# Optimization experiments

Measured on AMD Instinct MI355X. Metric: run time of the kernel, lower is better.

Reference implementation:

```python
import jax, jax.numpy as jnp
import numpy as np


def setup_inputs() -> dict:
    key = jax.random.key(0)
    ks = jax.random.split(key, 5)
    B, S, H = 64, 1024, 1024
    scale = 1.0 / np.sqrt(H)
    return {
        "decoder_hidden": jax.random.normal(ks[0], (B, H), jnp.float32),
        "encoder_outputs": jax.random.normal(ks[1], (B, S, H), jnp.float32),
        "W1": jax.random.normal(ks[2], (H, H), jnp.float32) * scale,
        "W2": jax.random.normal(ks[3], (H, H), jnp.float32) * scale,
        "v": jax.random.normal(ks[4], (H,), jnp.float32) * scale,
    }


def reference(decoder_hidden, encoder_outputs, W1, W2, v):
    # W1 @ decoder_hidden: [B, H] computed once, broadcast over src_len
    dh_proj = jnp.einsum("bh,oh->bo", decoder_hidden, W1)          # [B, H]
    enc_proj = jnp.einsum("bsh,oh->bso", encoder_outputs, W2)      # [B, S, H]
    energy = jnp.tanh(dh_proj[:, None, :] + enc_proj)              # [B, S, H]
    scores = jnp.einsum("bsh,h->bs", energy, v)                    # [B, S]
    attention_weights = jax.nn.softmax(scores, axis=-1)            # [B, S]
    context = jnp.einsum("bs,bsh->bh", attention_weights, encoder_outputs)
    return (context, attention_weights)
```

## Files before the change

### kernel.cpp

```cpp
#include <hip/hip_runtime.h>
#include <hip/hip_bf16.h>
#include <cmath>

#define Hdim 1024
#define Bdim 64
#define Sdim 1024

typedef __attribute__((ext_vector_type(4))) float f32x4;
typedef __attribute__((ext_vector_type(8))) short s16x8;
typedef __attribute__((ext_vector_type(4))) unsigned int u32x4;

static __device__ __forceinline__ unsigned short f2bf(float f) {
  unsigned int u = __builtin_bit_cast(unsigned int, f);
  unsigned int r = (u + 0x7fffu + ((u >> 16) & 1u)) >> 16;
  return (unsigned short)r;
}

static __device__ __forceinline__ float bf2f(unsigned short u) {
  return __builtin_bit_cast(float, (unsigned int)u << 16);
}

#define TANH_C 2.885390081777927f


static __device__ __forceinline__ void stage_rows64(const float* __restrict__ src,
                                                    unsigned short* As, int tid) {
  #pragma unroll 4
  for (int i = 0; i < 32; ++i) {
    int c = tid + i * 256;
    int row = c >> 7;
    int k8 = (c & 127) << 3;
    const float4* p = reinterpret_cast<const float4*>(src + row * Hdim + k8);
    float4 a = p[0];
    float4 b = p[1];
    union { unsigned short us[8]; u32x4 v; } pk;
    pk.us[0] = f2bf(a.x); pk.us[1] = f2bf(a.y); pk.us[2] = f2bf(a.z); pk.us[3] = f2bf(a.w);
    pk.us[4] = f2bf(b.x); pk.us[5] = f2bf(b.y); pk.us[6] = f2bf(b.z); pk.us[7] = f2bf(b.w);
    int idx = row * Hdim + (k8 ^ ((row & 7) << 3));
    *reinterpret_cast<u32x4*>(&As[idx]) = pk.v;
  }
}

static __device__ __forceinline__ s16x8 lda_full(const unsigned short* As, int row, int k) {
  int idx = row * Hdim + (k ^ ((row & 7) << 3));
  return *reinterpret_cast<const s16x8*>(&As[idx]);
}

static __device__ __forceinline__ s16x8 ldb_g(const unsigned short* __restrict__ Wb,
                                              const float* __restrict__ Wf,
                                              int use_bf, int o, int k) {
  if (use_bf) {
    return *reinterpret_cast<const s16x8*>(&Wb[o * Hdim + k]);
  } else {
    const float4* p = reinterpret_cast<const float4*>(Wf + o * Hdim + k);
    float4 a = p[0];
    float4 b = p[1];
    union { unsigned short us[8]; s16x8 v; } pk;
    pk.us[0] = f2bf(a.x); pk.us[1] = f2bf(a.y); pk.us[2] = f2bf(a.z); pk.us[3] = f2bf(a.w);
    pk.us[4] = f2bf(b.x); pk.us[5] = f2bf(b.y); pk.us[6] = f2bf(b.z); pk.us[7] = f2bf(b.w);
    return pk.v;
  }
}

__global__ void cast_bf16_kernel(const float* __restrict__ src,
                                 unsigned short* __restrict__ dst) {
  int i = blockIdx.x * 256 + threadIdx.x;
  const float4* p = reinterpret_cast<const float4*>(src) + i * 2;
  float4 a = p[0];
  float4 b = p[1];
  union { unsigned short us[8]; u32x4 v; } pk;
  pk.us[0] = f2bf(a.x); pk.us[1] = f2bf(a.y); pk.us[2] = f2bf(a.z); pk.us[3] = f2bf(a.w);
  pk.us[4] = f2bf(b.x); pk.us[5] = f2bf(b.y); pk.us[6] = f2bf(b.z); pk.us[7] = f2bf(b.w);
  *reinterpret_cast<u32x4*>(dst + i * 8) = pk.v;
}

__global__ __launch_bounds__(256, 1) void proj_kernel(
    const float* __restrict__ dh, const float* __restrict__ W1f,
    const unsigned short* __restrict__ W1b, float* __restrict__ out, int use_bf) {
  __shared__ unsigned short As[64 * Hdim];
  int tid = threadIdx.x;
  stage_rows64(dh, As, tid);
  __syncthreads();
  int w = tid >> 6, lane = tid & 63;
  int lo = lane & 15, hi = lane >> 4;
  int o = blockIdx.x * 16 + lo;
  f32x4 acc = {0.f, 0.f, 0.f, 0.f};
  for (int k0 = 0; k0 < Hdim; k0 += 32) {
    int k = k0 + hi * 8;
    s16x8 bfrag = ldb_g(W1b, W1f, use_bf, o, k);
    s16x8 afrag = lda_full(As, w * 16 + lo, k);
    acc = __builtin_amdgcn_mfma_f32_16x16x32_bf16(afrag, bfrag, acc, 0, 0, 0);
  }
  #pragma unroll
  for (int r = 0; r < 4; ++r)
    out[(w * 16 + hi * 4 + r) * Hdim + o] = acc[r];
}

#define SBM 256
#define SBN 256
#define SBK 64

__global__ __launch_bounds__(512, 2) void score_mfma_kernel(
    const unsigned short* __restrict__ encb,
    const unsigned short* __restrict__ W2b,
    const float* __restrict__ dhp, const float* __restrict__ v,
    float* __restrict__ scores) {
  __shared__ unsigned short As[3][SBM * SBK];
  __shared__ unsigned short Bs[2][SBN * SBK];
  int tid = threadIdx.x;
  int bid = blockIdx.x;
  int swz = (bid & 7) * 128 + (bid >> 3);
  int mp = swz >> 2;
  int np = swz & 3;
  int row0 = mp * SBM;
  int b = row0 >> 10;
  int w = tid >> 6, lane = tid & 63;
  int wr = w >> 2, wc = w & 3;
  int lo = lane & 15, hi = lane >> 4;

  const unsigned short* gA[4];
  const unsigned short* gB[4];
  #pragma unroll
  for (int i = 0; i < 4; ++i) {
    int d = i * 512 + tid;
    int row = d >> 3, c = d & 7;
    int gc = c ^ (row & 7);
    gA[i] = encb + (size_t)(row0 + row) * Hdim + gc * 8;
    gB[i] = W2b + (size_t)(np * SBN + row) * Hdim + gc * 8;
  }

  auto STAGE_A = [&](int t, int s) {
    #pragma unroll
    for (int i = 0; i < 4; ++i) {
      int dwv = i * 512 + w * 64;
      __builtin_amdgcn_global_load_lds(
          (const __attribute__((address_space(1))) unsigned int*)(gA[i] + t * SBK),
          (__attribute__((address_space(3))) unsigned int*)(&As[s][dwv * 8]), 16, 0, 0);
    }
  };
  auto STAGE_B = [&](int t, int s) {
    #pragma unroll
    for (int i = 0; i < 4; ++i) {
      int dwv = i * 512 + w * 64;
      __builtin_amdgcn_global_load_lds(
          (const __attribute__((address_space(1))) unsigned int*)(gB[i] + t * SBK),
          (__attribute__((address_space(3))) unsigned int*)(&Bs[s][dwv * 8]), 16, 0, 0);
    }
  };

  f32x4 acc[8][4] = {};

  STAGE_A(0, 0); STAGE_B(0, 0);
  STAGE_A(1, 1); STAGE_B(1, 1);
  STAGE_A(2, 2);
  asm volatile("s_waitcnt vmcnt(12)" ::: "memory");
  __builtin_amdgcn_s_barrier();
  asm volatile("" ::: "memory");

  int xorA = (lo & 7) << 4;

  #pragma unroll
  for (int t = 0; t < 16; ++t) {
    if (t >= 1 && t + 1 < 16) STAGE_B(t + 1, (t + 1) & 1);
    if (t >= 1 && t + 2 < 16) STAGE_A(t + 2, (t + 2) % 3);

    const char* Ab = (const char*)As[t % 3];
    const char* Bb = (const char*)Bs[t & 1];
    __builtin_amdgcn_s_setprio(1);
    #pragma unroll
    for (int ks = 0; ks < 2; ++ks) {
      int kb = ks * 64 + hi * 16;
      s16x8 af[8], bf[4];
      #pragma unroll
      for (int m = 0; m < 8; ++m) {
        int row = wr * 128 + m * 16 + lo;
        af[m] = *reinterpret_cast<const s16x8*>(Ab + row * 128 + (kb ^ xorA));
      }
      #pragma unroll
      for (int n = 0; n < 4; ++n) {
        int row = wc * 64 + n * 16 + lo;
        bf[n] = *reinterpret_cast<const s16x8*>(Bb + row * 128 + (kb ^ xorA));
      }
      #pragma unroll
      for (int m = 0; m < 8; ++m)
        #pragma unroll
        for (int n = 0; n < 4; ++n)
          acc[m][n] = __builtin_amdgcn_mfma_f32_16x16x32_bf16(af[m], bf[n], acc[m][n], 0, 0, 0);
    }
    __builtin_amdgcn_s_setprio(0);
    if (t <= 13) {
      asm volatile("s_waitcnt vmcnt(4)" ::: "memory");
    } else {
      asm volatile("s_waitcnt vmcnt(0)" ::: "memory");
    }
    __builtin_amdgcn_s_barrier();
    asm volatile("" ::: "memory");
  }

  float psum[8][4] = {};
  #pragma unroll
  for (int n = 0; n < 4; ++n) {
    int o = np * SBN + wc * 64 + n * 16 + lo;
    float dv = dhp[b * Hdim + o];
    float vv = v[o];
    float vv2 = 2.f * vv;
    #pragma unroll
    for (int m = 0; m < 8; ++m)
      #pragma unroll
      for (int r = 0; r < 4; ++r) {
        float x = acc[m][n][r] + dv;
        float e2 = __builtin_amdgcn_exp2f(x * TANH_C);
        float rc = __builtin_amdgcn_rcpf(1.f + e2);
        psum[m][r] += vv - vv2 * rc;
      }
  }
  #pragma unroll
  for (int mask = 1; mask < 16; mask <<= 1)
    #pragma unroll
    for (int m = 0; m < 8; ++m)
      #pragma unroll
      for (int r = 0; r < 4; ++r)
        psum[m][r] += __shfl_xor(psum[m][r], mask, 64);
  if (lo == 0) {
    #pragma unroll
    for (int m = 0; m < 8; ++m)
      #pragma unroll
      for (int r = 0; r < 4; ++r)
        atomicAdd(&scores[row0 + wr * 128 + m * 16 + hi * 4 + r], psum[m][r]);
  }
}

#define BKt 64

__global__ __launch_bounds__(256, 3) void score_kernel(
    const float* __restrict__ enc, const float* __restrict__ W2f,
    const unsigned short* __restrict__ W2b, const float* __restrict__ dhp,
    const float* __restrict__ v, float* __restrict__ scores, int use_bf) {
  __shared__ unsigned short As[64 * BKt];
  int tid = threadIdx.x;
  int bid = blockIdx.x;
  int f = (bid & 7) * 512 + (bid >> 3);
  int rg = f >> 2;
  int oc = f & 3;
  int row0 = rg * 64;
  int b = row0 >> 10;
  int w = tid >> 6, lane = tid & 63;
  int lo = lane & 15, hi = lane >> 4;
  int n0 = oc * 256 + w * 64;

  const unsigned short* pB[4];
  const float* pBf[4];
  #pragma unroll
  for (int n = 0; n < 4; ++n) {
    int o = n0 + n * 16 + lo;
    pB[n]  = W2b + (size_t)o * Hdim + hi * 8;
    pBf[n] = W2f + (size_t)o * Hdim + hi * 8;
  }

  f32x4 acc[4][4] = {};

  for (int t = 0; t < 16; ++t) {
    int k0 = t * BKt;
    __syncthreads();
    #pragma unroll
    for (int cc = 0; cc < 2; ++cc) {
      int c = tid + cc * 256;
      int row = c >> 3;
      int j = c & 7;
      const float4* p = reinterpret_cast<const float4*>(
          enc + (size_t)(row0 + row) * Hdim + k0 + j * 8);
      float4 a = p[0];
      float4 bb = p[1];
      union { unsigned short us[8]; u32x4 v4; } pk;
      pk.us[0] = f2bf(a.x);  pk.us[1] = f2bf(a.y);  pk.us[2] = f2bf(a.z);  pk.us[3] = f2bf(a.w);
      pk.us[4] = f2bf(bb.x); pk.us[5] = f2bf(bb.y); pk.us[6] = f2bf(bb.z); pk.us[7] = f2bf(bb.w);
      int idx = row * BKt + ((j * 8) ^ ((row & 7) << 3));
      *reinterpret_cast<u32x4*>(&As[idx]) = pk.v4;
    }
    __syncthreads();

    #pragma unroll
    for (int ks = 0; ks < 2; ++ks) {
      s16x8 bfrag[4];
      #pragma unroll
      for (int n = 0; n < 4; ++n) {
        if (use_bf) {
          bfrag[n] = *reinterpret_cast<const s16x8*>(pB[n] + ks * 32);
        } else {
          const float4* p = reinterpret_cast<const float4*>(pBf[n] + ks * 32);
          float4 a = p[0];
          float4 bb = p[1];
          union { unsigned short us[8]; s16x8 v4; } pk;
          pk.us[0] = f2bf(a.x);  pk.us[1] = f2bf(a.y);  pk.us[2] = f2bf(a.z);  pk.us[3] = f2bf(a.w);
          pk.us[4] = f2bf(bb.x); pk.us[5] = f2bf(bb.y); pk.us[6] = f2bf(bb.z); pk.us[7] = f2bf(bb.w);
          bfrag[n] = pk.v4;
        }
      }
      #pragma unroll
      for (int m = 0; m < 4; ++m) {
        int kk = ks * 32 + hi * 8;
        s16x8 afrag = *reinterpret_cast<const s16x8*>(
            &As[(m * 16 + lo) * BKt + (kk ^ ((lo & 7) << 3))]);
        #pragma unroll
        for (int n = 0; n < 4; ++n)
          acc[m][n] = __builtin_amdgcn_mfma_f32_16x16x32_bf16(afrag, bfrag[n], acc[m][n], 0, 0, 0);
      }
    }
    #pragma unroll
    for (int n = 0; n < 4; ++n) { pB[n] += BKt; pBf[n] += BKt; }
  }

  float psum[4][4] = {};
  #pragma unroll
  for (int n = 0; n < 4; ++n) {
    int o = n0 + n * 16 + lo;
    float dv = dhp[b * Hdim + o];
    float vv = v[o];
    float vv2 = 2.f * vv;
    #pragma unroll
    for (int m = 0; m < 4; ++m)
      #pragma unroll
      for (int r = 0; r < 4; ++r) {
        float x = acc[m][n][r] + dv;
        float e2 = __builtin_amdgcn_exp2f(x * TANH_C);
        float rc = __builtin_amdgcn_rcpf(1.f + e2);
        psum[m][r] += vv - vv2 * rc;
      }
  }
  #pragma unroll
  for (int mask = 1; mask < 16; mask <<= 1)
    #pragma unroll
    for (int m = 0; m < 4; ++m)
      #pragma unroll
      for (int r = 0; r < 4; ++r)
        psum[m][r] += __shfl_xor(psum[m][r], mask, 64);
  if (lo == 0) {
    #pragma unroll
    for (int m = 0; m < 4; ++m)
      #pragma unroll
      for (int r = 0; r < 4; ++r)
        atomicAdd(&scores[row0 + m * 16 + hi * 4 + r], psum[m][r]);
  }
}

__global__ __launch_bounds__(256, 1) void softmax_kernel(float* __restrict__ attn) {
  __shared__ float redm[4];
  __shared__ float reds[4];
  int b = blockIdx.x, tid = threadIdx.x;
  float4 x = *reinterpret_cast<float4*>(attn + b * Sdim + tid * 4);
  float m = fmaxf(fmaxf(x.x, x.y), fmaxf(x.z, x.w));
  #pragma unroll
  for (int mask = 1; mask < 64; mask <<= 1) m = fmaxf(m, __shfl_xor(m, mask, 64));
  if ((tid & 63) == 0) redm[tid >> 6] = m;
  __syncthreads();
  m = fmaxf(fmaxf(redm[0], redm[1]), fmaxf(redm[2], redm[3]));
  float4 e;
  e.x = expf(x.x - m); e.y = expf(x.y - m); e.z = expf(x.z - m); e.w = expf(x.w - m);
  float s = e.x + e.y + e.z + e.w;
  #pragma unroll
  for (int mask = 1; mask < 64; mask <<= 1) s += __shfl_xor(s, mask, 64);
  if ((tid & 63) == 0) reds[tid >> 6] = s;
  __syncthreads();
  s = reds[0] + reds[1] + reds[2] + reds[3];
  float inv = 1.f / s;
  e.x *= inv; e.y *= inv; e.z *= inv; e.w *= inv;
  *reinterpret_cast<float4*>(attn + b * Sdim + tid * 4) = e;
}

__global__ __launch_bounds__(256, 1) void context_bf_kernel(
    const unsigned short* __restrict__ encb, const float* __restrict__ attn,
    float* __restrict__ ctx) {
  int b = blockIdx.x >> 4;
  int chunk = blockIdx.x & 15;
  int tid = threadIdx.x;
  int h0 = tid * 4;
  const unsigned short* ebase = encb + ((size_t)(b * Sdim + chunk * 64)) * Hdim + h0;
  const float* abase = attn + b * Sdim + chunk * 64;
  float4 acc = {0.f, 0.f, 0.f, 0.f};
  #pragma unroll 4
  for (int s = 0; s < 64; ++s) {
    float wgt = abase[s];
    ushort4 ev = *reinterpret_cast<const ushort4*>(ebase + (size_t)s * Hdim);
    acc.x += wgt * bf2f(ev.x);
    acc.y += wgt * bf2f(ev.y);
    acc.z += wgt * bf2f(ev.z);
    acc.w += wgt * bf2f(ev.w);
  }
  float* c = ctx + b * Hdim + h0;
  atomicAdd(c + 0, acc.x);
  atomicAdd(c + 1, acc.y);
  atomicAdd(c + 2, acc.z);
  atomicAdd(c + 3, acc.w);
}

__global__ __launch_bounds__(256, 1) void context_kernel(
    const float* __restrict__ enc, const float* __restrict__ attn,
    float* __restrict__ ctx) {
  int b = blockIdx.x >> 3;
  int chunk = blockIdx.x & 7;
  int tid = threadIdx.x;
  int h0 = tid * 4;
  const float* ebase = enc + ((size_t)(b * Sdim + chunk * 128)) * Hdim + h0;
  const float* abase = attn + b * Sdim + chunk * 128;
  float4 acc = {0.f, 0.f, 0.f, 0.f};
  #pragma unroll 4
  for (int s = 0; s < 128; ++s) {
    float wgt = abase[s];
    float4 ev = *reinterpret_cast<const float4*>(ebase + (size_t)s * Hdim);
    acc.x += wgt * ev.x; acc.y += wgt * ev.y; acc.z += wgt * ev.z; acc.w += wgt * ev.w;
  }
  float* c = ctx + b * Hdim + h0;
  atomicAdd(c + 0, acc.x);
  atomicAdd(c + 1, acc.y);
  atomicAdd(c + 2, acc.z);
  atomicAdd(c + 3, acc.w);
}

extern "C" void kernel_launch(void* const* d_in, const int* in_sizes, int n_in,
                              void* d_out, int out_size, void* d_ws, size_t ws_size,
                              hipStream_t stream) {
  const float* dh  = (const float*)d_in[0];
  const float* enc = (const float*)d_in[1];
  const float* W1  = (const float*)d_in[2];
  const float* W2  = (const float*)d_in[3];
  const float* v   = (const float*)d_in[4];
  float* out_ctx  = (float*)d_out;
  float* out_attn = out_ctx + Bdim * Hdim;

  int use_bf = (ws_size >= 4ull * 1024 * 1024) ? 1 : 0;
  int big_ws = (ws_size >= 133ull * 1024 * 1024) ? 1 : 0;
  unsigned short* W1b  = (unsigned short*)d_ws;
  unsigned short* W2b  = W1b + 1024 * 1024;
  unsigned short* encb = W2b + 1024 * 1024;

  if (use_bf) {
    cast_bf16_kernel<<<512, 256, 0, stream>>>(W1, W1b);
    cast_bf16_kernel<<<512, 256, 0, stream>>>(W2, W2b);
  }
  if (big_ws) {
    cast_bf16_kernel<<<32768, 256, 0, stream>>>(enc, encb);
  }

  proj_kernel<<<64, 256, 0, stream>>>(dh, W1, W1b, out_ctx, use_bf);

  hipMemsetAsync(out_attn, 0, (size_t)Bdim * Sdim * sizeof(float), stream);
  if (big_ws) {
    score_mfma_kernel<<<1024, 512, 0, stream>>>(encb, W2b, out_ctx, v, out_attn);
  } else {
    score_kernel<<<4096, 256, 0, stream>>>(enc, W2, W2b, out_ctx, v, out_attn, use_bf);
  }

  softmax_kernel<<<Bdim, 256, 0, stream>>>(out_attn);

  hipMemsetAsync(out_ctx, 0, (size_t)Bdim * Hdim * sizeof(float), stream);
  if (big_ws) {
    context_bf_kernel<<<1024, 256, 0, stream>>>(encb, out_attn, out_ctx);
  } else {
    context_kernel<<<512, 256, 0, stream>>>(enc, out_attn, out_ctx);
  }
}
```

Before: 303.0 us.

## Restructure score GEMM into 8-phase ping-pong schedule with quadrant tiling

Rewrites the main loop of the bf16 MFMA score kernel. Each warp's output tile is split into four quadrants, and each K-tile is processed in four phases that interleave partial global-to-LDS loads with LDS fragment reads and a barrier. The A buffer drops from triple to double buffering, and launch bounds go from 2 to 1 block per CU, which gives more registers but lowers occupancy. The aim is finer-grained overlap of memory and MFMA work, at the cost of more barriers per tile.

```diff
diff --git a/kernel.cpp b/kernel.cpp
--- a/kernel.cpp
+++ b/kernel.cpp
@@ -100,12 +100,12 @@
 #define SBN 256
 #define SBK 64
 
-__global__ __launch_bounds__(512, 2) void score_mfma_kernel(
+__global__ __launch_bounds__(512, 1) void score_mfma_kernel(
     const unsigned short* __restrict__ encb,
     const unsigned short* __restrict__ W2b,
     const float* __restrict__ dhp, const float* __restrict__ v,
     float* __restrict__ scores) {
-  __shared__ unsigned short As[3][SBM * SBK];
+  __shared__ unsigned short As[2][SBM * SBK];
   __shared__ unsigned short Bs[2][SBN * SBK];
   int tid = threadIdx.x;
   int bid = blockIdx.x;
@@ -117,116 +117,128 @@
   int w = tid >> 6, lane = tid & 63;
   int wr = w >> 2, wc = w & 3;
   int lo = lane & 15, hi = lane >> 4;
-
-  const unsigned short* gA[4];
-  const unsigned short* gB[4];
-  #pragma unroll
-  for (int i = 0; i < 4; ++i) {
-    int d = i * 512 + tid;
-    int row = d >> 3, c = d & 7;
-    int gc = c ^ (row & 7);
-    gA[i] = encb + (size_t)(row0 + row) * Hdim + gc * 8;
-    gB[i] = W2b + (size_t)(np * SBN + row) * Hdim + gc * 8;
-  }
-
-  auto STAGE_A = [&](int t, int s) {
-    #pragma unroll
-    for (int i = 0; i < 4; ++i) {
-      int dwv = i * 512 + w * 64;
-      __builtin_amdgcn_global_load_lds(
-          (const __attribute__((address_space(1))) unsigned int*)(gA[i] + t * SBK),
-          (__attribute__((address_space(3))) unsigned int*)(&As[s][dwv * 8]), 16, 0, 0);
-    }
+  int xorv = (lo & 7) << 4;
+
+  int srow = tid >> 3;
+  int gc = (tid & 7) ^ (srow & 7);
+  const unsigned short* gA0 = encb + (size_t)(row0 + srow) * Hdim + gc * 8;
+  const unsigned short* gB0 = W2b + (size_t)(np * SBN + srow) * Hdim + gc * 8;
+
+  auto SA = [&](int g, int t, int s) {
+    __builtin_amdgcn_global_load_lds(
+        (const __attribute__((address_space(1))) unsigned int*)(gA0 + (size_t)g * 64 * Hdim + t * SBK),
+        (__attribute__((address_space(3))) unsigned int*)(&As[s][(g * 512 + w * 64) * 8]), 16, 0, 0);
   };
-  auto STAGE_B = [&](int t, int s) {
-    #pragma unroll
-    for (int i = 0; i < 4; ++i) {
-      int dwv = i * 512 + w * 64;
-      __builtin_amdgcn_global_load_lds(
-          (const __attribute__((address_space(1))) unsigned int*)(gB[i] + t * SBK),
-          (__attribute__((address_space(3))) unsigned int*)(&Bs[s][dwv * 8]), 16, 0, 0);
-    }
+  auto SB = [&](int g, int t, int s) {
+    __builtin_amdgcn_global_load_lds(
+        (const __attribute__((address_space(1))) unsigned int*)(gB0 + (size_t)g * 64 * Hdim + t * SBK),
+        (__attribute__((address_space(3))) unsigned int*)(&Bs[s][(g * 512 + w * 64) * 8]), 16, 0, 0);
   };
 
-  f32x4 acc[8][4] = {};
-
-  STAGE_A(0, 0); STAGE_B(0, 0);
-  STAGE_A(1, 1); STAGE_B(1, 1);
-  STAGE_A(2, 2);
-  asm volatile("s_waitcnt vmcnt(12)" ::: "memory");
+  f32x4 acc[2][2][4][2] = {};
+  s16x8 af[2][4][2];
+  s16x8 bf[2][2];
+
+  SA(0, 0, 0); SB(0, 0, 0);
+  SA(1, 0, 0); SB(1, 0, 0);
+  SA(2, 0, 0); SA(3, 0, 0);
+  SB(2, 0, 0); SB(3, 0, 0);
+  asm volatile("s_waitcnt vmcnt(4)" ::: "memory");
   __builtin_amdgcn_s_barrier();
   asm volatile("" ::: "memory");
 
-  int xorA = (lo & 7) << 4;
-
-  #pragma unroll
-  for (int t = 0; t < 16; ++t) {
-    if (t >= 1 && t + 1 < 16) STAGE_B(t + 1, (t + 1) & 1);
-    if (t >= 1 && t + 2 < 16) STAGE_A(t + 2, (t + 2) % 3);
-
-    const char* Ab = (const char*)As[t % 3];
-    const char* Bb = (const char*)Bs[t & 1];
-    __builtin_amdgcn_s_setprio(1);
-    #pragma unroll
-    for (int ks = 0; ks < 2; ++ks) {
-      int kb = ks * 64 + hi * 16;
-      s16x8 af[8], bf[4];
-      #pragma unroll
-      for (int m = 0; m < 8; ++m) {
-        int row = wr * 128 + m * 16 + lo;
-        af[m] = *reinterpret_cast<const s16x8*>(Ab + row * 128 + (kb ^ xorA));
+  for (int it = 0; it < 8; ++it) {
+    int t1 = 2 * it + 1;
+    int t2 = (it < 7) ? 2 * it + 2 : 15;
+    #pragma unroll
+    for (int p = 0; p < 8; ++p) {
+      const int grp = p >> 2;
+      const int q = p & 3;
+      const int mh = (q == 0 || q == 3) ? 0 : 1;
+      const int nh = q >> 1;
+      const int rs = grp;
+      const int ss = grp ^ 1;
+      const int st = grp ? t2 : t1;
+
+      if (q == 0)      { SA(0, st, ss); SB(0, st, ss); }
+      else if (q == 1) { SA(1, st, ss); SB(1, st, ss); }
+      else if (q == 2) { SA(2, st, ss); SA(3, st, ss); }
+      else             { SB(2, st, ss); SB(3, st, ss); }
+
+      const char* Ab = (const char*)As[rs];
+      const char* Bb = (const char*)Bs[rs];
+      if (q == 0 || q == 1) {
+        #pragma unroll
+        for (int m = 0; m < 4; ++m)
+          #pragma unroll
+          for (int ks = 0; ks < 2; ++ks)
+            af[mh][m][ks] = *reinterpret_cast<const s16x8*>(
+                Ab + (mh * 128 + wr * 64 + m * 16 + lo) * 128 + ((ks * 64 + hi * 16) ^ xorv));
       }
-      #pragma unroll
-      for (int n = 0; n < 4; ++n) {
-        int row = wc * 64 + n * 16 + lo;
-        bf[n] = *reinterpret_cast<const s16x8*>(Bb + row * 128 + (kb ^ xorA));
+      if (q == 0 || q == 2) {
+        #pragma unroll
+        for (int n = 0; n < 2; ++n)
+          #pragma unroll
+          for (int ks = 0; ks < 2; ++ks)
+            bf[n][ks] = *reinterpret_cast<const s16x8*>(
+                Bb + (nh * 128 + wc * 32 + n * 16 + lo) * 128 + ((ks * 64 + hi * 16) ^ xorv));
       }
-      #pragma unroll
-      for (int m = 0; m < 8; ++m)
-        #pragma unroll
-        for (int n = 0; n < 4; ++n)
-          acc[m][n] = __builtin_amdgcn_mfma_f32_16x16x32_bf16(af[m], bf[n], acc[m][n], 0, 0, 0);
+
+      asm volatile("s_waitcnt vmcnt(4)" ::: "memory");
+      __builtin_amdgcn_s_barrier();
+      asm volatile("" ::: "memory");
+
+      __builtin_amdgcn_s_setprio(1);
+      #pragma unroll
+      for (int ks = 0; ks < 2; ++ks)
+        #pragma unroll
+        for (int m = 0; m < 4; ++m)
+          #pragma unroll
+          for (int n = 0; n < 2; ++n)
+            acc[mh][nh][m][n] = __builtin_amdgcn_mfma_f32_16x16x32_bf16(
+                af[mh][m][ks], bf[n][ks], acc[mh][nh][m][n], 0, 0, 0);
+      __builtin_amdgcn_s_setprio(0);
     }
-    __builtin_amdgcn_s_setprio(0);
-    if (t <= 13) {
-      asm volatile("s_waitcnt vmcnt(4)" ::: "memory");
-    } else {
-      asm volatile("s_waitcnt vmcnt(0)" ::: "memory");
+  }
+
+  float psum[2][4][4] = {};
+  #pragma unroll
+  for (int nh = 0; nh < 2; ++nh)
+    #pragma unroll
+    for (int n = 0; n < 2; ++n) {
+      int o = np * SBN + nh * 128 + wc * 32 + n * 16 + lo;
+      float dv = dhp[b * Hdim + o];
+      float vv = v[o];
+      float vv2 = 2.f * vv;
+      #pragma unroll
+      for (int mh = 0; mh < 2; ++mh)
+        #pragma unroll
+        for (int m = 0; m < 4; ++m)
+          #pragma unroll
+          for (int r = 0; r < 4; ++r) {
+            float x = acc[mh][nh][m][n][r] + dv;
+            float e2 = __builtin_amdgcn_exp2f(x * TANH_C);
+            float rc = __builtin_amdgcn_rcpf(1.f + e2);
+            psum[mh][m][r] += vv - vv2 * rc;
+          }
     }
-    __builtin_amdgcn_s_barrier();
-    asm volatile("" ::: "memory");
-  }
-
-  float psum[8][4] = {};
-  #pragma unroll
-  for (int n = 0; n < 4; ++n) {
-    int o = np * SBN + wc * 64 + n * 16 + lo;
-    float dv = dhp[b * Hdim + o];
-    float vv = v[o];
-    float vv2 = 2.f * vv;
-    #pragma unroll
-    for (int m = 0; m < 8; ++m)
-      #pragma unroll
-      for (int r = 0; r < 4; ++r) {
-        float x = acc[m][n][r] + dv;
-        float e2 = __builtin_amdgcn_exp2f(x * TANH_C);
-        float rc = __builtin_amdgcn_rcpf(1.f + e2);
-        psum[m][r] += vv - vv2 * rc;
-      }
-  }
   #pragma unroll
   for (int mask = 1; mask < 16; mask <<= 1)
     #pragma unroll
-    for (int m = 0; m < 8; ++m)
-      #pragma unroll
-      for (int r = 0; r < 4; ++r)
-        psum[m][r] += __shfl_xor(psum[m][r], mask, 64);
+    for (int mh = 0; mh < 2; ++mh)
+      #pragma unroll
+      for (int m = 0; m < 4; ++m)
+        #pragma unroll
+        for (int r = 0; r < 4; ++r)
+          psum[mh][m][r] += __shfl_xor(psum[mh][m][r], mask, 64);
   if (lo == 0) {
     #pragma unroll
-    for (int m = 0; m < 8; ++m)
-      #pragma unroll
-      for (int r = 0; r < 4; ++r)
-        atomicAdd(&scores[row0 + wr * 128 + m * 16 + hi * 4 + r], psum[m][r]);
+    for (int mh = 0; mh < 2; ++mh)
+      #pragma unroll
+      for (int m = 0; m < 4; ++m)
+        #pragma unroll
+        for (int r = 0; r < 4; ++r)
+          atomicAdd(&scores[row0 + mh * 128 + wr * 64 + m * 16 + hi * 4 + r], psum[mh][m][r]);
   }
 }
 
```

Result: faster. 290.2 us (-4.2%).
